# Kernel tuning notes

Measured on AMD Instinct MI355X. Metric: run time of the kernel, lower is better.

## Reference

```python
import jax, jax.numpy as jnp
import numpy as np

# Standard bitsandbytes NF4 codebook (16 values)
NF4_CODE = jnp.array([
    -1.0, -0.6961928009986877, -0.5250730514526367, -0.39491748809814453,
    -0.28444138169288635, -0.18477343022823334, -0.09105003625154495, 0.0,
    0.07958029955625534, 0.16093020141124725, 0.24611230194568634,
    0.33791524171829224, 0.44070982933044434, 0.5626170039176941,
    0.7229568362236023, 1.0], dtype=jnp.float32)

BLOCKSIZE = 64
IN_FEATURES = 4096
OUT_FEATURES = 11008


def setup_inputs() -> dict:
    key = jax.random.key(0)
    k1, k2, k3, k4 = jax.random.split(key, 4)
    x = jax.random.normal(k1, (4, 2048, IN_FEATURES), dtype=jnp.float32)
    weight_q = jax.random.randint(k2, (OUT_FEATURES, IN_FEATURES), 0, 16, dtype=jnp.int32)
    absmax = jax.random.uniform(k3, (OUT_FEATURES, IN_FEATURES // BLOCKSIZE), dtype=jnp.float32)
    bias = jax.random.normal(k4, (OUT_FEATURES,), dtype=jnp.float32)
    return {"x": x, "weight_q": weight_q, "absmax": absmax, "bias": bias}


def reference(x, weight_q, absmax, bias):
    out_f, in_f = weight_q.shape
    # Blockwise NF4 dequantization: code lookup * per-block absmax scale
    w_code = NF4_CODE[weight_q]                                   # [O, I]
    w_blocks = w_code.reshape(out_f, in_f // BLOCKSIZE, BLOCKSIZE)
    w = (w_blocks * absmax[:, :, None]).reshape(out_f, in_f)      # [O, I]
    # Linear: y = x @ W^T + b
    y = jnp.einsum('bsi,oi->bso', x, w) + bias
    return y
```

## Files before the change

### kernel.cpp

```cpp
#include <hip/hip_runtime.h>
#include <hip/hip_bf16.h>
#include <stdint.h>

typedef __attribute__((ext_vector_type(8))) short short8;
typedef __attribute__((ext_vector_type(8))) unsigned short ushort8;
typedef __attribute__((ext_vector_type(4))) float f32x4;

#define K_DIM 4096
#define N_DIM 11008
#define M_DIM 8192
#define BM 256
#define BN 256
#define BK 64
#define TILES (K_DIM / BK)

__constant__ float c_nf4[16] = {
    -1.0f, -0.6961928009986877f, -0.5250730514526367f, -0.39491748809814453f,
    -0.28444138169288635f, -0.18477343022823334f, -0.09105003625154495f, 0.0f,
    0.07958029955625534f, 0.16093020141124725f, 0.24611230194568634f,
    0.33791524171829224f, 0.44070982933044434f, 0.5626170039176941f,
    0.7229568362236023f, 1.0f};

__device__ __forceinline__ unsigned short f2bf(float f) {
    uint32_t u = __float_as_uint(f);
    u += 0x7fffu + ((u >> 16) & 1u);
    return (unsigned short)(u >> 16);
}

__global__ __launch_bounds__(256) void nf4_dequant_w(const int* __restrict__ q,
                                                     const float* __restrict__ absmax,
                                                     unsigned short* __restrict__ w) {
    __shared__ float lut[16];
    if (threadIdx.x < 16) lut[threadIdx.x] = c_nf4[threadIdx.x];
    __syncthreads();
    size_t t = (size_t)blockIdx.x * 256 + threadIdx.x;
    const int4* q4 = (const int4*)q;
    int4 qa = q4[2 * t];
    int4 qb = q4[2 * t + 1];
    float s = absmax[t >> 3];
    ushort8 o;
    o[0] = f2bf(lut[qa.x & 15] * s);
    o[1] = f2bf(lut[qa.y & 15] * s);
    o[2] = f2bf(lut[qa.z & 15] * s);
    o[3] = f2bf(lut[qa.w & 15] * s);
    o[4] = f2bf(lut[qb.x & 15] * s);
    o[5] = f2bf(lut[qb.y & 15] * s);
    o[6] = f2bf(lut[qb.z & 15] * s);
    o[7] = f2bf(lut[qb.w & 15] * s);
    ((ushort8*)w)[t] = o;
}

__global__ __launch_bounds__(256) void x_to_bf16(const float* __restrict__ x,
                                                 unsigned short* __restrict__ xb) {
    size_t t = (size_t)blockIdx.x * 256 + threadIdx.x;
    const float4* x4 = (const float4*)x;
    float4 a = x4[2 * t];
    float4 b = x4[2 * t + 1];
    ushort8 o;
    o[0] = f2bf(a.x); o[1] = f2bf(a.y); o[2] = f2bf(a.z); o[3] = f2bf(a.w);
    o[4] = f2bf(b.x); o[5] = f2bf(b.y); o[6] = f2bf(b.z); o[7] = f2bf(b.w);
    ((ushort8*)xb)[t] = o;
}

#define STAGE_HALF(gbase, region, j, k0)                                    \
  do {                                                                      \
    _Pragma("unroll")                                                       \
    for (int _g = 0; _g < 2; ++_g) {                                        \
      const int _D = _g * 512 + tid;                \
      const int _r = (j) * 128 + (_D >> 3);                                 \
      const int _c = (_D & 7) ^ (_r & 7);                 \
      __builtin_amdgcn_global_load_lds(                                     \
          (const __attribute__((address_space(1))) void*)((gbase) +         \
              (size_t)_r * K_DIM + (k0) + _c * 8),                          \
          (__attribute__((address_space(3))) void*)((region) +              \
              ((j) * 1024 + _g * 512 + wave * 64) * 8),                     \
          16, 0, 0);                                                        \
    }                                                                       \
  } while (0)

#define READS(kksel)                                                        \
  do {                                                                      \
    _Pragma("unroll")                                                       \
    for (int mi = 0; mi < 8; ++mi)                                          \
      af[mi] = *(const short8*)(Ar + wm * 8192 + mi * 1024 + (roff ^ (kksel))); \
    _Pragma("unroll")                                                       \
    for (int ni = 0; ni < 4; ++ni)                                          \
      bf[ni] = *(const short8*)(Br + wn * 4096 + ni * 1024 + (roff ^ (kksel))); \
  } while (0)

#define MFMA32                                                              \
  do {                                                                      \
    _Pragma("unroll")                                                       \
    for (int mi = 0; mi < 8; ++mi) {                                        \
      _Pragma("unroll")                                                     \
      for (int ni = 0; ni < 4; ++ni)                                        \
        acc[mi][ni] = __builtin_amdgcn_mfma_f32_16x16x32_bf16(              \
            af[mi], bf[ni], acc[mi][ni], 0, 0, 0);                          \
    }                                                                       \
  } while (0)

__global__ __launch_bounds__(512, 2) void gemm256(const unsigned short* __restrict__ A,
                                                  const unsigned short* __restrict__ B,
                                                  const float* __restrict__ bias,
                                                  float* __restrict__ C) {
    __shared__ unsigned short As[2][BM * BK];
    __shared__ unsigned short Bs[2][BN * BK];

    const int tid  = threadIdx.x;
    const int wave = tid >> 6;
    const int lane = tid & 63;
    const int wm = wave >> 2;
    const int wn = wave & 3;
    const int lr = lane & 15;
    const int q  = lane >> 4;
    const int roff = lr * 64 + ((q ^ (lr & 7)) << 3);
    const int early = (wave < 2);

    const int nbn = N_DIM / BN;
    const int cpx = (int)gridDim.x >> 3;
    const int bid = (int)blockIdx.x;
    const int swz = (bid & 7) * cpx + (bid >> 3);
    const int bm = swz / nbn;
    const int bn = swz % nbn;

    const unsigned short* Ab = A + (size_t)bm * BM * K_DIM;
    const unsigned short* Bb = B + (size_t)bn * BN * K_DIM;

    f32x4 acc[8][4];
#pragma unroll
    for (int i = 0; i < 8; ++i)
#pragma unroll
        for (int j = 0; j < 4; ++j)
#pragma unroll
            for (int v = 0; v < 4; ++v) acc[i][j][v] = 0.0f;

    STAGE_HALF(Ab, &As[0][0], 0, 0); STAGE_HALF(Bb, &Bs[0][0], 0, 0);
    STAGE_HALF(Ab, &As[0][0], 1, 0); STAGE_HALF(Bb, &Bs[0][0], 1, 0);
    asm volatile("s_waitcnt vmcnt(4)" ::: "memory");
    asm volatile("s_barrier" ::: "memory");

#pragma unroll 1
    for (int t = 0; t < TILES; ++t) {
        const int p = t & 1;
        const unsigned short* Ar = &As[p][0];
        const unsigned short* Br = &Bs[p][0];
        unsigned short* Aw = &As[p ^ 1][0];
        unsigned short* Bw = &Bs[p ^ 1][0];
        int ts = t + 1; if (ts >= TILES) ts = 0;
        const int k0s = ts * BK;

        short8 af[8], bf[4];

        STAGE_HALF(Ab, Aw, 0, k0s);
        STAGE_HALF(Bb, Bw, 0, k0s);
        if (early) READS(0);
        asm volatile("s_waitcnt vmcnt(4)" ::: "memory");
        asm volatile("s_barrier" ::: "memory");
        if (!early) READS(0);
        STAGE_HALF(Ab, Aw, 1, k0s);
        STAGE_HALF(Bb, Bw, 1, k0s);

        __builtin_amdgcn_s_setprio(1);
        MFMA32;
        READS(32);
        MFMA32;
        __builtin_amdgcn_s_setprio(0);

        asm volatile("s_waitcnt vmcnt(4)" ::: "memory");
        asm volatile("s_barrier" ::: "memory");
    }
    asm volatile("s_waitcnt vmcnt(0)" ::: "memory");

    const int row0 = bm * BM + wm * 128 + (q << 2);
    const int col0 = bn * BN + wn * 64 + lr;
#pragma unroll
    for (int ni = 0; ni < 4; ++ni) {
        const int col = col0 + ni * 16;
        const float bv = bias[col];
#pragma unroll
        for (int mi = 0; mi < 8; ++mi) {
#pragma unroll
            for (int v = 0; v < 4; ++v) {
                C[(size_t)(row0 + mi * 16 + v) * N_DIM + col] = acc[mi][ni][v] + bv;
            }
        }
    }
}

extern "C" void kernel_launch(void* const* d_in, const int* in_sizes, int n_in,
                              void* d_out, int out_size, void* d_ws, size_t ws_size,
                              hipStream_t stream) {
    const float* x    = (const float*)d_in[0];
    const int*   wq   = (const int*)d_in[1];
    const float* am   = (const float*)d_in[2];
    const float* bias = (const float*)d_in[3];
    float* out = (float*)d_out;

    const size_t w_elems = (size_t)N_DIM * K_DIM;
    const size_t x_elems = (size_t)M_DIM * K_DIM;
    const size_t need = (w_elems + x_elems) * sizeof(unsigned short);
    if (ws_size < need) return;

    unsigned short* wbf = (unsigned short*)d_ws;
    unsigned short* xbf = wbf + w_elems;

    nf4_dequant_w<<<(int)(w_elems / 8 / 256), 256, 0, stream>>>(wq, am, wbf);
    x_to_bf16<<<(int)(x_elems / 8 / 256), 256, 0, stream>>>(x, xbf);

    const int grid = (M_DIM / BM) * (N_DIM / BN);
    gemm256<<<grid, 512, 0, stream>>>(xbf, wbf, bias, out);
}
```

Baseline: 992.3 us.

## Split K-tiles into 32-wide LDS sub-buffers with finer-grained staged pipeline

Restructures the GEMM main loop so each 64-wide K tile is stored as two 32-wide LDS sub-buffers. Global-to-LDS loads for the next sub-tiles are interleaved with four smaller MFMA phases separated by barriers, and prefetch now runs up to two half-tiles ahead. The aim is to overlap memory traffic with compute more evenly and to cut register pressure by halving the A fragment count. In exchange it drops the XOR swizzle, so the 64-byte-row LDS layout may see bank conflicts, and it adds more barriers per tile.

```diff
diff --git a/kernel.cpp b/kernel.cpp
--- a/kernel.cpp
+++ b/kernel.cpp
@@ -62,49 +62,61 @@
     ((ushort8*)xb)[t] = o;
 }
 
-#define STAGE_HALF(gbase, region, j, k0)                                    \
-  do {                                                                      \
-    _Pragma("unroll")                                                       \
-    for (int _g = 0; _g < 2; ++_g) {                                        \
-      const int _D = _g * 512 + tid;                \
-      const int _r = (j) * 128 + (_D >> 3);                                 \
-      const int _c = (_D & 7) ^ (_r & 7);                 \
-      __builtin_amdgcn_global_load_lds(                                     \
-          (const __attribute__((address_space(1))) void*)((gbase) +         \
-              (size_t)_r * K_DIM + (k0) + _c * 8),                          \
-          (__attribute__((address_space(3))) void*)((region) +              \
-              ((j) * 1024 + _g * 512 + wave * 64) * 8),                     \
-          16, 0, 0);                                                        \
-    }                                                                       \
+#define STAGE_SUB(gbase, lds_sub, kcol0)                                      \
+  do {                                                                        \
+    _Pragma("unroll")                                                         \
+    for (int _g = 0; _g < 2; ++_g) {                                          \
+      const int _i = _g * 512 + tid;                             \
+      const int _r = _i >> 2;                                 \
+      const int _c = (_i & 3) << 3;                   \
+      __builtin_amdgcn_global_load_lds(                                       \
+          (const __attribute__((address_space(1))) void*)((gbase) +           \
+              (size_t)_r * K_DIM + (kcol0) + _c),                             \
+          (__attribute__((address_space(3))) void*)((lds_sub) +               \
+              (_g * 512 + wave * 64) * 8),                                    \
+          16, 0, 0);                                                          \
+    }                                                                         \
   } while (0)
 
-#define READS(kksel)                                                        \
-  do {                                                                      \
-    _Pragma("unroll")                                                       \
-    for (int mi = 0; mi < 8; ++mi)                                          \
-      af[mi] = *(const short8*)(Ar + wm * 8192 + mi * 1024 + (roff ^ (kksel))); \
-    _Pragma("unroll")                                                       \
-    for (int ni = 0; ni < 4; ++ni)                                          \
-      bf[ni] = *(const short8*)(Br + wn * 4096 + ni * 1024 + (roff ^ (kksel))); \
+#define DS_A4(sub, rbase)                                                     \
+  af[0] = *(const short8*)((sub) + ((rbase) +  0 + lr) * 32 + q8);            \
+  af[1] = *(const short8*)((sub) + ((rbase) + 16 + lr) * 32 + q8);            \
+  af[2] = *(const short8*)((sub) + ((rbase) + 32 + lr) * 32 + q8);            \
+  af[3] = *(const short8*)((sub) + ((rbase) + 48 + lr) * 32 + q8);
+
+#define DS_B4(sub)                                                            \
+  bfr[0] = *(const short8*)((sub) + (wn * 64 +  0 + lr) * 32 + q8);           \
+  bfr[1] = *(const short8*)((sub) + (wn * 64 + 16 + lr) * 32 + q8);           \
+  bfr[2] = *(const short8*)((sub) + (wn * 64 + 32 + lr) * 32 + q8);           \
+  bfr[3] = *(const short8*)((sub) + (wn * 64 + 48 + lr) * 32 + q8);
+
+#define MFMA16(MI0)                                                           \
+  do {                                                                        \
+    _Pragma("unroll")                                                         \
+    for (int _m = 0; _m < 4; ++_m) {                                          \
+      _Pragma("unroll")                                                       \
+      for (int _n = 0; _n < 4; ++_n)                                          \
+        acc[(MI0) + _m][_n] = __builtin_amdgcn_mfma_f32_16x16x32_bf16(        \
+            af[_m], bfr[_n], acc[(MI0) + _m][_n], 0, 0, 0);                   \
+    }                                                                         \
   } while (0)
 
-#define MFMA32                                                              \
-  do {                                                                      \
-    _Pragma("unroll")                                                       \
-    for (int mi = 0; mi < 8; ++mi) {                                        \
-      _Pragma("unroll")                                                     \
-      for (int ni = 0; ni < 4; ++ni)                                        \
-        acc[mi][ni] = __builtin_amdgcn_mfma_f32_16x16x32_bf16(              \
-            af[mi], bf[ni], acc[mi][ni], 0, 0, 0);                          \
-    }                                                                       \
-  } while (0)
+#define MIDBAR_MFMA(MI0)                                                      \
+  asm volatile("s_barrier" ::: "memory");                                     \
+  asm volatile("s_waitcnt lgkmcnt(0)" ::: "memory");                          \
+  __builtin_amdgcn_sched_barrier(0);                                          \
+  __builtin_amdgcn_s_setprio(1);                                              \
+  MFMA16(MI0);                                                                \
+  __builtin_amdgcn_s_setprio(0);                                              \
+  __builtin_amdgcn_sched_barrier(0);                                          \
+  asm volatile("s_barrier" ::: "memory");
 
 __global__ __launch_bounds__(512, 2) void gemm256(const unsigned short* __restrict__ A,
                                                   const unsigned short* __restrict__ B,
                                                   const float* __restrict__ bias,
                                                   float* __restrict__ C) {
-    __shared__ unsigned short As[2][BM * BK];
-    __shared__ unsigned short Bs[2][BN * BK];
+    __shared__ unsigned short As[2][2][BM * 32];
+    __shared__ unsigned short Bs[2][2][BN * 32];
 
     const int tid  = threadIdx.x;
     const int wave = tid >> 6;
@@ -112,9 +124,7 @@
     const int wm = wave >> 2;
     const int wn = wave & 3;
     const int lr = lane & 15;
-    const int q  = lane >> 4;
-    const int roff = lr * 64 + ((q ^ (lr & 7)) << 3);
-    const int early = (wave < 2);
+    const int q8 = (lane >> 4) << 3;
 
     const int nbn = N_DIM / BN;
     const int cpx = (int)gridDim.x >> 3;
@@ -134,44 +144,48 @@
 #pragma unroll
             for (int v = 0; v < 4; ++v) acc[i][j][v] = 0.0f;
 
-    STAGE_HALF(Ab, &As[0][0], 0, 0); STAGE_HALF(Bb, &Bs[0][0], 0, 0);
-    STAGE_HALF(Ab, &As[0][0], 1, 0); STAGE_HALF(Bb, &Bs[0][0], 1, 0);
+    STAGE_SUB(Ab, &As[0][0][0], 0);
+    STAGE_SUB(Bb, &Bs[0][0][0], 0);
+    STAGE_SUB(Ab, &As[0][1][0], 32);
+    STAGE_SUB(Bb, &Bs[0][1][0], 32);
+    STAGE_SUB(Ab, &As[1][0][0], BK);
+    STAGE_SUB(Bb, &Bs[1][0][0], BK);
     asm volatile("s_waitcnt vmcnt(4)" ::: "memory");
     asm volatile("s_barrier" ::: "memory");
+
+    short8 af[4], bfr[4];
 
 #pragma unroll 1
     for (int t = 0; t < TILES; ++t) {
         const int p = t & 1;
-        const unsigned short* Ar = &As[p][0];
-        const unsigned short* Br = &Bs[p][0];
-        unsigned short* Aw = &As[p ^ 1][0];
-        unsigned short* Bw = &Bs[p ^ 1][0];
-        int ts = t + 1; if (ts >= TILES) ts = 0;
-        const int k0s = ts * BK;
-
-        short8 af[8], bf[4];
-
-        STAGE_HALF(Ab, Aw, 0, k0s);
-        STAGE_HALF(Bb, Bw, 0, k0s);
-        if (early) READS(0);
+        int t1 = t + 1; if (t1 >= TILES) t1 -= TILES;
+        int t2 = t + 2; if (t2 >= TILES) t2 -= TILES;
+        const int p1 = t1 & 1;
+        const int p2 = t2 & 1;
+
+        DS_A4(&As[p][0][0], wm * 128);
+        DS_B4(&Bs[p][0][0]);
+        STAGE_SUB(Ab, &As[p1][1][0], t1 * BK + 32);
+        MIDBAR_MFMA(0);
+
+        DS_A4(&As[p][0][0], wm * 128 + 64);
+        STAGE_SUB(Bb, &Bs[p1][1][0], t1 * BK + 32);
         asm volatile("s_waitcnt vmcnt(4)" ::: "memory");
-        asm volatile("s_barrier" ::: "memory");
-        if (!early) READS(0);
-        STAGE_HALF(Ab, Aw, 1, k0s);
-        STAGE_HALF(Bb, Bw, 1, k0s);
-
-        __builtin_amdgcn_s_setprio(1);
-        MFMA32;
-        READS(32);
-        MFMA32;
-        __builtin_amdgcn_s_setprio(0);
-
+        MIDBAR_MFMA(4);
+
+        DS_A4(&As[p][1][0], wm * 128);
+        DS_B4(&Bs[p][1][0]);
+        STAGE_SUB(Ab, &As[p2][0][0], t2 * BK);
+        MIDBAR_MFMA(0);
+
+        DS_A4(&As[p][1][0], wm * 128 + 64);
+        STAGE_SUB(Bb, &Bs[p2][0][0], t2 * BK);
         asm volatile("s_waitcnt vmcnt(4)" ::: "memory");
-        asm volatile("s_barrier" ::: "memory");
+        MIDBAR_MFMA(4);
     }
     asm volatile("s_waitcnt vmcnt(0)" ::: "memory");
 
-    const int row0 = bm * BM + wm * 128 + (q << 2);
+    const int row0 = bm * BM + wm * 128 + ((lane >> 4) << 2);
     const int col0 = bn * BN + wn * 64 + lr;
 #pragma unroll
     for (int ni = 0; ni < 4; ++ni) {
```

New measurement: 945.3 us. -4.7%, faster.
